# Performance work log

Measured on AMD Instinct MI355X. Metric: run time of the kernel, lower is better.

## Reference

```python
import jax, jax.numpy as jnp
import numpy as np

E = 2048   # embedding_size
H = 2048   # hidden_size
B = 512    # batch
OUT = 2    # output_size (coords)


def setup_inputs() -> dict:
    key = jax.random.key(0)
    ks = jax.random.split(key, 11)
    s = 0.02
    return {
        "embedding": jax.random.normal(ks[0], (B, E), dtype=jnp.float32),
        "max_seq_length": 256,
        "W_embed": jax.random.normal(ks[1], (H, E), dtype=jnp.float32) * s,
        "b_embed": jnp.zeros((H,), dtype=jnp.float32),
        "W_ih": jax.random.normal(ks[2], (4 * H, OUT), dtype=jnp.float32) * s,
        "b_ih": jnp.zeros((4 * H,), dtype=jnp.float32),
        "W_hh": jax.random.normal(ks[3], (4 * H, H), dtype=jnp.float32) * s,
        "b_hh": jnp.zeros((4 * H,), dtype=jnp.float32),
        "W_out": jax.random.normal(ks[4], (OUT, H), dtype=jnp.float32) * s,
        "b_out": jnp.zeros((OUT,), dtype=jnp.float32),
        "W_stop": jax.random.normal(ks[5], (1, H), dtype=jnp.float32) * s,
        "b_stop": jnp.zeros((1,), dtype=jnp.float32),
    }


def reference(embedding, max_seq_length, W_embed, b_embed, W_ih, b_ih,
              W_hh, b_hh, W_out, b_out, W_stop, b_stop):
    # h_0 from embedding head (num_layers == 1)
    h0 = embedding @ W_embed.T + b_embed          # (B, H)
    c0 = jnp.zeros_like(h0)
    x0 = jnp.zeros((embedding.shape[0], OUT), dtype=embedding.dtype)

    def step(carry, _):
        h, c, x = carry
        gates = x @ W_ih.T + b_ih + h @ W_hh.T + b_hh    # (B, 4H)
        i, f, g, o = jnp.split(gates, 4, axis=-1)         # torch gate order i,f,g,o
        c = jax.nn.sigmoid(f) * c + jax.nn.sigmoid(i) * jnp.tanh(g)
        h = jax.nn.sigmoid(o) * jnp.tanh(c)
        coord = h @ W_out.T + b_out                        # (B, 2)
        stop = jax.nn.sigmoid(h @ W_stop.T + b_stop)       # (B, 1)
        return (h, c, coord), (coord, stop)

    _, (coords, stops) = jax.lax.scan(step, (h0, c0, x0), xs=None,
                                      length=max_seq_length)
    outputs = jnp.transpose(coords, (1, 0, 2))     # (B, T, 2)
    stop_probs = jnp.transpose(stops, (1, 0, 2))   # (B, T, 1)
    return outputs, stop_probs
```

## Files before the change

### kernel.cpp

```cpp
#include <hip/hip_runtime.h>
#include <stdint.h>

#define E_DIM 2048
#define H_DIM 2048
#define B_DIM 512
#define T_DIM 256
#define G4H   8192

typedef unsigned short u16;
typedef __attribute__((ext_vector_type(8))) short bf16x8;
typedef __attribute__((ext_vector_type(4))) float f32x4;

__device__ inline u16 f2b(float f) {
  union { float f; uint32_t i; } v; v.f = f;
  uint32_t u = v.i;
  return (u16)((u + 0x7FFFu + ((u >> 16) & 1u)) >> 16);
}
__device__ inline float b2f(u16 u) {
  union { uint32_t i; float f; } v; v.i = ((uint32_t)u) << 16; return v.f;
}

__global__ __launch_bounds__(256) void convert_bf16(const float* __restrict__ s,
                                                    u16* __restrict__ d, int n4) {
  int i = blockIdx.x * 256 + threadIdx.x;
  if (i < n4) {
    float4 f = ((const float4*)s)[i];
    ushort4 o;
    o.x = f2b(f.x); o.y = f2b(f.y); o.z = f2b(f.z); o.w = f2b(f.w);
    ((ushort4*)d)[i] = o;
  }
}

__global__ __launch_bounds__(256) void build_weff(const float* __restrict__ W,
                                                  const float* __restrict__ W_ih,
                                                  const float* __restrict__ W_out,
                                                  u16* __restrict__ Wz) {
  int id = blockIdx.x * 256 + threadIdx.x;
  int lane = id & 63;
  int k32  = (id >> 6) & 63;
  int n16  = id >> 12;
  int np = n16 * 16 + (lane & 15);
  int k  = k32 * 32 + (lane >> 4) * 8;
  int g = np & 3, jrow = np >> 2;
  int src = g * H_DIM + jrow;
  float wi0 = W_ih[src * 2 + 0], wi1 = W_ih[src * 2 + 1];
  const float* sw = W + (size_t)src * H_DIM + k;
  u16 out[8];
  for (int j = 0; j < 8; ++j) {
    float v = sw[j] + wi0 * W_out[k + j] + wi1 * W_out[H_DIM + k + j];
    out[j] = f2b(v);
  }
  u16* dst = Wz + (size_t)id * 8;
  *(ushort4*)(dst) = *(ushort4*)&out[0];
  *(ushort4*)(dst + 4) = *(ushort4*)&out[4];
}

__global__ __launch_bounds__(256) void build_epi(const float* __restrict__ b_ih,
                                                 const float* __restrict__ b_hh,
                                                 const float* __restrict__ W_ih,
                                                 const float* __restrict__ b_out,
                                                 float* __restrict__ epi) {
  int np = blockIdx.x * 256 + threadIdx.x;
  int src = (np & 3) * H_DIM + (np >> 2);
  float wi0 = W_ih[src * 2 + 0], wi1 = W_ih[src * 2 + 1];
  float4 e;
  e.x = b_ih[src] + b_hh[src] + b_out[0] * wi0 + b_out[1] * wi1;
  e.y = wi0;
  e.z = wi1;
  e.w = 0.f;
  ((float4*)epi)[np] = e;
}

#define BM 64
#define BN 128
#define BK 32
__global__ __launch_bounds__(256) void gemm_bt(const u16* __restrict__ A,
                                               const u16* __restrict__ Bm,
                                               float* __restrict__ C,
                                               int M, int N, int K) {
  __shared__ u16 sA[BM * BK];
  __shared__ u16 sB[BN * BK];
  const int t = threadIdx.x;
  const int bm0 = blockIdx.y * BM, bn0 = blockIdx.x * BN;
  const int wave = t >> 6, lane = t & 63;
  const int wm = (wave >> 1) * 32, wn = (wave & 1) * 64;
  const int r16 = lane & 15, quad = lane >> 4;

  f32x4 acc[2][4];
  const f32x4 z = {0.f, 0.f, 0.f, 0.f};
  for (int i = 0; i < 2; ++i)
    for (int j = 0; j < 4; ++j) acc[i][j] = z;

  const int arow = t >> 2, acg = t & 3;

  for (int k0 = 0; k0 < K; k0 += BK) {
    __syncthreads();
    *(uint4*)&sA[arow * BK + acg * 8] =
        *(const uint4*)&A[(size_t)(bm0 + arow) * K + k0 + acg * 8];
    for (int i = 0; i < 2; ++i) {
      int c = t + 256 * i;
      int row = c >> 2, cg = c & 3;
      *(uint4*)&sB[row * BK + cg * 8] =
          *(const uint4*)&Bm[(size_t)(bn0 + row) * K + k0 + cg * 8];
    }
    __syncthreads();
    bf16x8 af[2], bfr[4];
    for (int mt = 0; mt < 2; ++mt)
      af[mt] = *(const bf16x8*)&sA[(wm + mt * 16 + r16) * BK + quad * 8];
    for (int nt = 0; nt < 4; ++nt)
      bfr[nt] = *(const bf16x8*)&sB[(wn + nt * 16 + r16) * BK + quad * 8];
    for (int mt = 0; mt < 2; ++mt)
      for (int nt = 0; nt < 4; ++nt)
        acc[mt][nt] = __builtin_amdgcn_mfma_f32_16x16x32_bf16(af[mt], bfr[nt],
                                                              acc[mt][nt], 0, 0, 0);
  }
  for (int mt = 0; mt < 2; ++mt)
    for (int nt = 0; nt < 4; ++nt) {
      int row = bm0 + wm + mt * 16 + quad * 4;
      int col = bn0 + wn + nt * 16 + r16;
      for (int r = 0; r < 4; ++r)
        C[(size_t)(row + r) * N + col] = acc[mt][nt][r];
    }
}

__global__ __launch_bounds__(256) void init_state(const float* __restrict__ h0pre,
                                                  const float* __restrict__ b_embed,
                                                  u16* __restrict__ h,
                                                  float* __restrict__ c,
                                                  float* __restrict__ xzero) {
  int idx = blockIdx.x * 256 + threadIdx.x;
  int bg = idx >> 11, k = idx & (H_DIM - 1);
  float v = h0pre[idx] + b_embed[k];
  size_t chunk = (((size_t)(bg >> 4)) * 64 + (k >> 5)) * 64 + ((k >> 3) & 3) * 16 + (bg & 15);
  size_t pos = chunk * 8 + (k & 7);
  h[pos] = f2b(v);
  c[pos] = 0.f;
  if (idx < B_DIM * 2) xzero[idx] = 0.f;
}

__global__ __launch_bounds__(64) void calc_xcorr(const float* __restrict__ h0pre,
                                                 const float* __restrict__ b_embed,
                                                 const float* __restrict__ W_out,
                                                 const float* __restrict__ b_out,
                                                 float* __restrict__ xc) {
  int m = blockIdx.x, ln = threadIdx.x;
  float s0 = 0.f, s1 = 0.f;
  for (int k = ln; k < H_DIM; k += 64) {
    float hv = h0pre[(size_t)m * H_DIM + k] + b_embed[k];
    s0 += hv * W_out[k];
    s1 += hv * W_out[H_DIM + k];
  }
  for (int off = 32; off > 0; off >>= 1) {
    s0 += __shfl_down(s0, off);
    s1 += __shfl_down(s1, off);
  }
  if (ln == 0) {
    xc[m * 2 + 0] = -(s0 + b_out[0]);
    xc[m * 2 + 1] = -(s1 + b_out[1]);
  }
}

__global__ __launch_bounds__(256) void init_out(const float* __restrict__ b_out,
                                                const float* __restrict__ b_stop,
                                                float* __restrict__ coords,
                                                float* __restrict__ stops) {
  int i = blockIdx.x * 256 + threadIdx.x;
  coords[i * 2 + 0] = b_out[0];
  coords[i * 2 + 1] = b_out[1];
  stops[i] = b_stop[0];
}

__global__ __launch_bounds__(256) void finalize_stops(float* __restrict__ stops) {
  int i = blockIdx.x * 256 + threadIdx.x;
  stops[i] = 1.f / (1.f + __expf(-stops[i]));
}

__global__ __launch_bounds__(512) void gemm_lstm(const u16* __restrict__ hA,
                                                 const u16* __restrict__ Wz,
                                                 const float* __restrict__ epi,
                                                 const float* __restrict__ x,
                                                 float* __restrict__ c,
                                                 u16* __restrict__ h_out,
                                                 const float* __restrict__ W_out,
                                                 const float* __restrict__ W_stop,
                                                 float* __restrict__ coords,
                                                 float* __restrict__ stops,
                                                 int trow) {
  __shared__ char smem[33792];
  float* gt   = (float*)smem;
  float* comb = (float*)smem;

  const int bid = blockIdx.x;
  const int nt = (bid & 7) * 8 + ((bid >> 3) & 7);
  const int mt = bid >> 6;
  const int bm0 = mt * 128;

  const int t = threadIdx.x, wv = t >> 6, ln = t & 63;
  const int q = wv & 3, kh = wv >> 2;
  const int qm = q & 1, qn = q >> 1;
  const int r16 = ln & 15, quad = ln >> 4;

  const u16* pA[4];
  const u16* pB[4];
  for (int i = 0; i < 4; ++i) {
    pA[i] = hA + (size_t)((bm0 >> 4) + qm * 4 + i) * 32768 +
            (size_t)(kh * 32) * 512 + ln * 8;
    pB[i] = Wz + (size_t)(nt * 8 + qn * 4 + i) * 32768 +
            (size_t)(kh * 32) * 512 + ln * 8;
  }

  f32x4 acc[4][4];
  const f32x4 z = {0.f, 0.f, 0.f, 0.f};
  for (int i = 0; i < 4; ++i)
    for (int j = 0; j < 4; ++j) acc[i][j] = z;

  bf16x8 af[2][4], bf[2][4];
  for (int i = 0; i < 4; ++i) {
    af[0][i] = *(const bf16x8*)(pA[i]);
    bf[0][i] = *(const bf16x8*)(pB[i]);
  }

#pragma unroll 2
  for (int kk = 0; kk < 32; ++kk) {
    const int s = kk & 1;
    if (kk + 1 < 32) {
      const int sp = s ^ 1;
      for (int i = 0; i < 4; ++i) {
        af[sp][i] = *(const bf16x8*)(pA[i] + (size_t)(kk + 1) * 512);
        bf[sp][i] = *(const bf16x8*)(pB[i] + (size_t)(kk + 1) * 512);
      }
    }
    for (int mi = 0; mi < 4; ++mi)
      for (int ni = 0; ni < 4; ++ni)
        acc[mi][ni] = __builtin_amdgcn_mfma_f32_16x16x32_bf16(af[s][mi], bf[s][ni],
                                                              acc[mi][ni], 0, 0, 0);
  }

  for (int r = 0; r < 2; ++r) {
    __syncthreads();
    if (kh == 1 && qn == r) {
      float* dst = comb + qm * 4096;
      for (int mi = 0; mi < 4; ++mi)
        for (int ni = 0; ni < 4; ++ni)
          *(f32x4*)&dst[((mi * 4 + ni) * 64 + ln) * 4] = acc[mi][ni];
    }
    __syncthreads();
    if (kh == 0 && qn == r) {
      const float* src = comb + qm * 4096;
      for (int mi = 0; mi < 4; ++mi)
        for (int ni = 0; ni < 4; ++ni) {
          f32x4 p = *(const f32x4*)&src[((mi * 4 + ni) * 64 + ln) * 4];
          acc[mi][ni] += p;
        }
    }
  }

  for (int half = 0; half < 2; ++half) {
    __syncthreads();
    if (kh == 0 && qm == half) {
      for (int mi = 0; mi < 4; ++mi)
        for (int ni = 0; ni < 4; ++ni) {
          int row = mi * 16 + quad * 4;
          int col = qn * 64 + ni * 16 + r16;
          for (int r = 0; r < 4; ++r)
            gt[(row + r) * 132 + col] = acc[mi][ni][r];
        }
    }
    __syncthreads();
    if (kh == half) {
      const int lrow = q * 16 + r16;
      const int bg = bm0 + half * 64 + lrow;
      const float x0 = x[bg * 2 + 0], x1 = x[bg * 2 + 1];
      const size_t chunk = (((size_t)(bg >> 4)) * 64 + nt) * 64 + ln;
      const int hc0 = nt * 32 + quad * 8;
      float cv[8]; u16 hv[8];
      float s0 = 0.f, s1 = 0.f, s2 = 0.f;
      const float4* epi4 = (const float4*)epi;
      for (int j = 0; j < 8; ++j) {
        int col = quad * 32 + j * 4;
        float4 g4 = *(const float4*)&gt[lrow * 132 + col];
        float4 e0 = epi4[nt * 128 + col + 0];
        float4 e1 = epi4[nt * 128 + col + 1];
        float4 e2 = epi4[nt * 128 + col + 2];
        float4 e3 = epi4[nt * 128 + col + 3];
        float gi = g4.x + e0.x + x0 * e0.y + x1 * e0.z;
        float gf = g4.y + e1.x + x0 * e1.y + x1 * e1.z;
        float gg = g4.z + e2.x + x0 * e2.y + x1 * e2.z;
        float go = g4.w + e3.x + x0 * e3.y + x1 * e3.z;
        float si = 1.f / (1.f + __expf(-gi));
        float sf = 1.f / (1.f + __expf(-gf));
        float so = 1.f / (1.f + __expf(-go));
        float cn = sf * c[chunk * 8 + j] + si * tanhf(gg);
        cv[j] = cn;
        float hf = so * tanhf(cn);
        hv[j] = f2b(hf);
        s0 += hf * W_out[hc0 + j];
        s1 += hf * W_out[H_DIM + hc0 + j];
        s2 += hf * W_stop[hc0 + j];
      }
      *(float4*)&c[chunk * 8 + 0] = *(float4*)&cv[0];
      *(float4*)&c[chunk * 8 + 4] = *(float4*)&cv[4];
      *(ushort4*)&h_out[chunk * 8 + 0] = *(ushort4*)&hv[0];
      *(ushort4*)&h_out[chunk * 8 + 4] = *(ushort4*)&hv[4];
      s0 += __shfl_xor(s0, 16); s1 += __shfl_xor(s1, 16); s2 += __shfl_xor(s2, 16);
      s0 += __shfl_xor(s0, 32); s1 += __shfl_xor(s1, 32); s2 += __shfl_xor(s2, 32);
      if (quad == 0) {
        atomicAdd(&coords[((size_t)bg * T_DIM + trow) * 2 + 0], s0);
        atomicAdd(&coords[((size_t)bg * T_DIM + trow) * 2 + 1], s1);
        atomicAdd(&stops[(size_t)bg * T_DIM + trow], s2);
      }
    }
  }
}

extern "C" void kernel_launch(void* const* d_in, const int* in_sizes, int n_in,
                              void* d_out, int out_size, void* d_ws, size_t ws_size,
                              hipStream_t stream) {
  const float* embedding = (const float*)d_in[0];
  const float* W_embed   = (const float*)d_in[2];
  const float* b_embed   = (const float*)d_in[3];
  const float* W_ih      = (const float*)d_in[4];
  const float* b_ih      = (const float*)d_in[5];
  const float* W_hh      = (const float*)d_in[6];
  const float* b_hh      = (const float*)d_in[7];
  const float* W_out     = (const float*)d_in[8];
  const float* b_out     = (const float*)d_in[9];
  const float* W_stop    = (const float*)d_in[10];
  const float* b_stop    = (const float*)d_in[11];

  float* coords = (float*)d_out;
  float* stops  = (float*)d_out + (size_t)B_DIM * T_DIM * 2;

  char* ws = (char*)d_ws;
  u16* W_z     = (u16*)ws;   ws += (size_t)G4H * H_DIM * 2;
  u16* W_emb_b = (u16*)ws;   ws += (size_t)H_DIM * E_DIM * 2;
  u16* emb_b   = (u16*)ws;   ws += (size_t)B_DIM * E_DIM * 2;
  float* h0pre = (float*)ws; ws += (size_t)B_DIM * H_DIM * 4;
  float* epi   = (float*)ws; ws += (size_t)G4H * 4 * 4;
  float* cbuf  = (float*)ws; ws += (size_t)B_DIM * H_DIM * 4;
  u16* hbuf0   = (u16*)ws;   ws += (size_t)B_DIM * H_DIM * 2;
  u16* hbuf1   = (u16*)ws;   ws += (size_t)B_DIM * H_DIM * 2;
  float* xcorr = (float*)ws; ws += (size_t)B_DIM * 2 * 4;
  float* xzero = (float*)ws; ws += (size_t)B_DIM * 2 * 4;

  convert_bf16<<<(B_DIM * E_DIM / 4 + 255) / 256, 256, 0, stream>>>(embedding, emb_b, B_DIM * E_DIM / 4);
  convert_bf16<<<(H_DIM * E_DIM / 4 + 255) / 256, 256, 0, stream>>>(W_embed, W_emb_b, H_DIM * E_DIM / 4);
  build_weff<<<(G4H * H_DIM / 8) / 256, 256, 0, stream>>>(W_hh, W_ih, W_out, W_z);
  build_epi<<<G4H / 256, 256, 0, stream>>>(b_ih, b_hh, W_ih, b_out, epi);
  init_out<<<(B_DIM * T_DIM) / 256, 256, 0, stream>>>(b_out, b_stop, coords, stops);

  gemm_bt<<<dim3(H_DIM / BN, B_DIM / BM), 256, 0, stream>>>(emb_b, W_emb_b, h0pre,
                                                            B_DIM, H_DIM, E_DIM);
  init_state<<<(B_DIM * H_DIM) / 256, 256, 0, stream>>>(h0pre, b_embed, hbuf0, cbuf, xzero);
  calc_xcorr<<<B_DIM, 64, 0, stream>>>(h0pre, b_embed, W_out, b_out, xcorr);

  for (int t = 0; t < T_DIM; ++t) {
    u16* h_in  = (t & 1) ? hbuf1 : hbuf0;
    u16* h_out = (t & 1) ? hbuf0 : hbuf1;
    const float* xv = (t == 0) ? xcorr : xzero;
    gemm_lstm<<<256, 512, 0, stream>>>(h_in, W_z, epi, xv, cbuf, h_out,
                                       W_out, W_stop, coords, stops, t);
  }
  finalize_stops<<<(B_DIM * T_DIM) / 256, 256, 0, stream>>>(stops);
}
```

Measured before the change: 8.287 ms.

## Reorganize GEMM waves into 4-way split-K with larger per-wave M tiles

```diff
diff --git a/kernel.cpp b/kernel.cpp
--- a/kernel.cpp
+++ b/kernel.cpp
@@ -186,9 +186,9 @@
                                                  float* __restrict__ coords,
                                                  float* __restrict__ stops,
                                                  int trow) {
-  __shared__ char smem[33792];
-  float* gt   = (float*)smem;
-  float* comb = (float*)smem;
+  __shared__ char smem[131072];
+  float* cb = (float*)smem;
+  float* gt = (float*)smem;
 
   const int bid = blockIdx.x;
   const int nt = (bid & 7) * 8 + ((bid >> 3) & 7);
@@ -196,78 +196,83 @@
   const int bm0 = mt * 128;
 
   const int t = threadIdx.x, wv = t >> 6, ln = t & 63;
-  const int q = wv & 3, kh = wv >> 2;
-  const int qm = q & 1, qn = q >> 1;
+  const int wn2 = wv & 1, kq = wv >> 1;
   const int r16 = ln & 15, quad = ln >> 4;
 
-  const u16* pA[4];
+  const u16* pA[8];
   const u16* pB[4];
-  for (int i = 0; i < 4; ++i) {
-    pA[i] = hA + (size_t)((bm0 >> 4) + qm * 4 + i) * 32768 +
-            (size_t)(kh * 32) * 512 + ln * 8;
-    pB[i] = Wz + (size_t)(nt * 8 + qn * 4 + i) * 32768 +
-            (size_t)(kh * 32) * 512 + ln * 8;
-  }
-
-  f32x4 acc[4][4];
+  for (int i = 0; i < 8; ++i)
+    pA[i] = hA + (size_t)((bm0 >> 4) + i) * 32768 + (size_t)(kq * 16) * 512 + ln * 8;
+  for (int i = 0; i < 4; ++i)
+    pB[i] = Wz + (size_t)(nt * 8 + wn2 * 4 + i) * 32768 + (size_t)(kq * 16) * 512 + ln * 8;
+
+  f32x4 acc[8][4];
   const f32x4 z = {0.f, 0.f, 0.f, 0.f};
-  for (int i = 0; i < 4; ++i)
+  for (int i = 0; i < 8; ++i)
     for (int j = 0; j < 4; ++j) acc[i][j] = z;
 
-  bf16x8 af[2][4], bf[2][4];
-  for (int i = 0; i < 4; ++i) {
-    af[0][i] = *(const bf16x8*)(pA[i]);
-    bf[0][i] = *(const bf16x8*)(pB[i]);
-  }
+  bf16x8 af[2][8], bf[2][4];
+  for (int i = 0; i < 8; ++i) af[0][i] = *(const bf16x8*)(pA[i]);
+  for (int i = 0; i < 4; ++i) bf[0][i] = *(const bf16x8*)(pB[i]);
 
 #pragma unroll 2
-  for (int kk = 0; kk < 32; ++kk) {
-    const int s = kk & 1;
-    if (kk + 1 < 32) {
-      const int sp = s ^ 1;
-      for (int i = 0; i < 4; ++i) {
-        af[sp][i] = *(const bf16x8*)(pA[i] + (size_t)(kk + 1) * 512);
-        bf[sp][i] = *(const bf16x8*)(pB[i] + (size_t)(kk + 1) * 512);
-      }
-    }
-    for (int mi = 0; mi < 4; ++mi)
-      for (int ni = 0; ni < 4; ++ni)
-        acc[mi][ni] = __builtin_amdgcn_mfma_f32_16x16x32_bf16(af[s][mi], bf[s][ni],
+  for (int kk = 0; kk < 16; ++kk) {
+    const int cu = kk & 1;
+    if (kk < 15) {
+      const int nx = cu ^ 1;
+      const size_t off = (size_t)(kk + 1) * 512;
+      for (int i = 0; i < 8; ++i) af[nx][i] = *(const bf16x8*)(pA[i] + off);
+      for (int i = 0; i < 4; ++i) bf[nx][i] = *(const bf16x8*)(pB[i] + off);
+    }
+    for (int mi = 0; mi < 8; ++mi)
+      for (int ni = 0; ni < 4; ++ni)
+        acc[mi][ni] = __builtin_amdgcn_mfma_f32_16x16x32_bf16(af[cu][mi], bf[cu][ni],
                                                               acc[mi][ni], 0, 0, 0);
   }
 
-  for (int r = 0; r < 2; ++r) {
-    __syncthreads();
-    if (kh == 1 && qn == r) {
-      float* dst = comb + qm * 4096;
-      for (int mi = 0; mi < 4; ++mi)
-        for (int ni = 0; ni < 4; ++ni)
-          *(f32x4*)&dst[((mi * 4 + ni) * 64 + ln) * 4] = acc[mi][ni];
-    }
-    __syncthreads();
-    if (kh == 0 && qn == r) {
-      const float* src = comb + qm * 4096;
-      for (int mi = 0; mi < 4; ++mi)
-        for (int ni = 0; ni < 4; ++ni) {
-          f32x4 p = *(const f32x4*)&src[((mi * 4 + ni) * 64 + ln) * 4];
-          acc[mi][ni] += p;
-        }
-    }
+  if (kq >= 2) {
+    float* dst = cb + ((kq - 2) * 2 + wn2) * 8192;
+    for (int mi = 0; mi < 8; ++mi)
+      for (int ni = 0; ni < 4; ++ni)
+        *(f32x4*)&dst[((mi * 4 + ni) * 64 + ln) * 4] = acc[mi][ni];
+  }
+  __syncthreads();
+  if (kq < 2) {
+    const float* src = cb + (kq * 2 + wn2) * 8192;
+    for (int mi = 0; mi < 8; ++mi)
+      for (int ni = 0; ni < 4; ++ni)
+        acc[mi][ni] += *(const f32x4*)&src[((mi * 4 + ni) * 64 + ln) * 4];
+  }
+  __syncthreads();
+  if (kq == 1) {
+    float* dst = cb + wn2 * 8192;
+    for (int mi = 0; mi < 8; ++mi)
+      for (int ni = 0; ni < 4; ++ni)
+        *(f32x4*)&dst[((mi * 4 + ni) * 64 + ln) * 4] = acc[mi][ni];
+  }
+  __syncthreads();
+  if (kq == 0) {
+    const float* src = cb + wn2 * 8192;
+    for (int mi = 0; mi < 8; ++mi)
+      for (int ni = 0; ni < 4; ++ni)
+        acc[mi][ni] += *(const f32x4*)&src[((mi * 4 + ni) * 64 + ln) * 4];
   }
 
   for (int half = 0; half < 2; ++half) {
     __syncthreads();
-    if (kh == 0 && qm == half) {
+    if (wv < 2) {
       for (int mi = 0; mi < 4; ++mi)
         for (int ni = 0; ni < 4; ++ni) {
           int row = mi * 16 + quad * 4;
-          int col = qn * 64 + ni * 16 + r16;
+          int col = wn2 * 64 + ni * 16 + r16;
+          f32x4 v = acc[half * 4 + mi][ni];
           for (int r = 0; r < 4; ++r)
-            gt[(row + r) * 132 + col] = acc[mi][ni][r];
+            gt[(row + r) * 132 + col] = v[r];
         }
     }
     __syncthreads();
-    if (kh == half) {
+    if ((wv >> 2) == half) {
+      const int q = wv & 3;
       const int lrow = q * 16 + r16;
       const int bg = bm0 + half * 64 + lrow;
       const float x0 = x[bg * 2 + 0], x1 = x[bg * 2 + 1];
```

Measured after the change: 7.818 ms. -5.7%, faster.
